# Kernel tuning notes

Hardware: AMD Instinct MI355X
Metric: run time of the kernel (lower is better)

## Reference

```python
import jax, jax.numpy as jnp
import numpy as np

B, T, C, H = 4, 4096, 1024, 16


def setup_inputs() -> dict:
    key = jax.random.key(0)
    k1, k2, k3 = jax.random.split(key, 3)
    x = jax.random.normal(k1, (B, T, C), dtype=jnp.float32)
    # nn.Linear(d_model, 3*d_model, bias=False): weight shape [3C, C]
    W_qkv = jax.random.normal(k2, (3 * C, C), dtype=jnp.float32) * 0.02
    # output Linear(d_model, d_model): weight [C, C], bias [C]
    W_out = jax.random.normal(k3, (C, C), dtype=jnp.float32) * 0.02
    b_out = jnp.zeros((C,), dtype=jnp.float32)
    return {"x": x, "W_qkv": W_qkv, "W_out": W_out, "b_out": b_out}


def reference(x, W_qkv, W_out, b_out):
    Bs, Ts, Cs = x.shape
    dh = Cs // H
    scale = dh ** (-0.5)
    # qkv projection: [B,T,3C]
    qkv = x @ W_qkv.T
    q, k, v = jnp.split(qkv, 3, axis=-1)

    def to_heads(t):  # [B,T,C] -> [B,H,T,dh]
        return t.reshape(Bs, Ts, H, dh).transpose(0, 2, 1, 3)

    q, k, v = to_heads(q), to_heads(k), to_heads(v)
    # rfft over the sequence dim -> [B,H,F,dh], F = T//2+1 (complex64)
    q_f = jnp.fft.rfft(q, axis=-2)
    k_f = jnp.fft.rfft(k, axis=-2)
    # spectral score: sum over head_dim of conj(q)*k, real part -> [B,H,F]
    attn = jnp.sum(jnp.conj(q_f) * k_f, axis=-1).real * scale
    attn = jax.nn.softmax(attn, axis=-1)  # softmax over frequency bins
    v_f = jnp.fft.rfft(v, axis=-2)
    out = jnp.fft.irfft(attn[..., None] * v_f, n=Ts, axis=-2)  # [B,H,T,dh]
    out = out.transpose(0, 2, 1, 3).reshape(Bs, Ts, Cs)
    # output projection (dropout is identity in eval)
    return out @ W_out.T + b_out
```

## Files before the change

kernel.cpp:

```cpp
#include <hip/hip_runtime.h>
#include <math.h>

#define Bsz   4
#define Tsz   4096
#define Csz   1024
#define Hn    16
#define DHn   64
#define NTOT  (Bsz * Tsz)
#define M3    (3 * Csz)
#define Fn    2049
#define BHn   (Bsz * Hn)
#define HALFN 8192

typedef __bf16 bf16x8 __attribute__((ext_vector_type(8)));
typedef __bf16 bf16x4 __attribute__((ext_vector_type(4)));
typedef float  f32x4  __attribute__((ext_vector_type(4)));

#define VMCNT(n) asm volatile("s_waitcnt vmcnt(" #n ")" ::: "memory")
#define LGKM0    asm volatile("s_waitcnt lgkmcnt(0)" ::: "memory")

__device__ __forceinline__ void gload_lds16(const void* g, void* l) {
  __builtin_amdgcn_global_load_lds(
      (const __attribute__((address_space(1))) void*)g,
      (__attribute__((address_space(3))) void*)l, 16, 0, 0);
}

__global__ __launch_bounds__(256)
void cvt_hilo_kernel(const float4* __restrict__ in, bf16x4* __restrict__ hi,
                     bf16x4* __restrict__ lo, int n4) {
  int i = blockIdx.x * blockDim.x + threadIdx.x;
  if (i >= n4) return;
  float4 v = in[i];
  bf16x4 h, l;
  h[0] = (__bf16)v.x; h[1] = (__bf16)v.y; h[2] = (__bf16)v.z; h[3] = (__bf16)v.w;
  l[0] = (__bf16)(v.x - (float)h[0]);
  l[1] = (__bf16)(v.y - (float)h[1]);
  l[2] = (__bf16)(v.z - (float)h[2]);
  l[3] = (__bf16)(v.w - (float)h[3]);
  hi[i] = h;
  lo[i] = l;
}

__global__ __launch_bounds__(256)
void transpose_cvt_kernel(const float* __restrict__ src,
                          __bf16* __restrict__ hi, __bf16* __restrict__ lo) {
  __shared__ float tile[64][65];
  const int tid = threadIdx.x;
  const int n0 = blockIdx.x * 64;
  const int c0 = blockIdx.y * 64;
  const int col = tid & 63;
  const int row4 = tid >> 6;
#pragma unroll
  for (int i = 0; i < 16; ++i) {
    const int r = i * 4 + row4;
    tile[r][col] = src[(size_t)(c0 + r) * NTOT + n0 + col];
  }
  __syncthreads();
#pragma unroll
  for (int i = 0; i < 16; ++i) {
    const int n = i * 4 + row4;
    const float v = tile[col][n];
    const __bf16 h = (__bf16)v;
    const __bf16 l = (__bf16)(v - (float)h);
    hi[(size_t)(n0 + n) * Csz + c0 + col] = h;
    lo[(size_t)(n0 + n) * Csz + c0 + col] = l;
  }
}

template<int COLMAP>
__global__ __launch_bounds__(512, 2)
void gemm_8s(const __bf16* __restrict__ Ahi, const __bf16* __restrict__ Alo,
             const __bf16* __restrict__ Bhi, const __bf16* __restrict__ Blo,
             float* __restrict__ C, int ldC, int nbase,
             const float* __restrict__ bias) {
  __shared__ __align__(16) char lds[131072];

  const int tid  = threadIdx.x;
  const int wid  = tid >> 6;
  const int lane = tid & 63;
  const int wm = wid >> 2, wn = wid & 3;

  int bx = blockIdx.x, by = blockIdx.y;
  {
    const int gx = gridDim.x, gy = gridDim.y;
    const int nwg = gx * gy;
    if ((nwg & 7) == 0) {
      const int flat  = by * gx + bx;
      const int chunk = nwg >> 3;
      const int nf    = (flat & 7) * chunk + (flat >> 3);
      if (COLMAP) { bx = nf / gy; by = nf % gy; }
      else        { bx = nf % gx; by = nf / gx; }
    }
  }
  const int m0 = by * 256;
  const int n0 = bx * 256;

  const int r16 = lane & 15;
  const int kc  = lane >> 4;

  const int aq = (wid & 3) + ((wid & 4) ? 4 : 0);
  const int bq = ((wid & 3) << 1) + (wid >> 2);
  const __bf16* gAh = Ahi + (size_t)(m0 + (wid & 3) * 16 + ((wid & 4) ? 128 : 0) + r16) * Csz + kc * 8;
  const __bf16* gAl = Alo + (size_t)(m0 + (wid & 3) * 16 + ((wid & 4) ? 128 : 0) + r16) * Csz + kc * 8;
  const __bf16* gBh = Bhi + (size_t)(n0 + (wid & 3) * 64 + (wid >> 2) * 16 + r16) * Csz + kc * 8;
  const __bf16* gBl = Blo + (size_t)(n0 + (wid & 3) * 64 + (wid >> 2) * 16 + r16) * Csz + kc * 8;

  auto stA = [&](int h, int ts, char* slot) {
    const size_t o = (size_t)h * 64 * Csz + ts * 32;
    gload_lds16(gAh + o, slot + aq * 1024);
    gload_lds16(gAl + o, slot + 8192 + aq * 1024);
  };
  auto stB = [&](int h, int ts, char* slot) {
    const size_t o = (size_t)h * 32 * Csz + ts * 32;
    gload_lds16(gBh + o, slot + bq * 1024);
    gload_lds16(gBl + o, slot + 8192 + bq * 1024);
  };

  f32x4 acc[8][4];
#pragma unroll
  for (int i = 0; i < 8; ++i)
#pragma unroll
    for (int j = 0; j < 4; ++j) acc[i][j] = (f32x4)(0.f);

  stA(0, 0, lds);            stB(0, 0, lds + 16384);
  stB(1, 0, lds + 32768);    stA(1, 0, lds + 49152);
  stA(0, 1, lds + 65536);    stB(0, 1, lds + 81920);

#pragma unroll 1
  for (int t = 0; t < 32; ++t) {
    char* cur = lds + ((t & 1) << 16);
    char* nxt = lds + (((t & 1) ^ 1) << 16);
    bf16x8 ah[4], al[4], bh[4], bl[4];

    if (t < 31) { VMCNT(8); } else { VMCNT(4); }
    __builtin_amdgcn_s_barrier();
#pragma unroll
    for (int f = 0; f < 4; ++f) {
      const int off = (wm * 4 + f) * 1024 + lane * 16;
      ah[f] = *(const bf16x8*)(cur + off);
      al[f] = *(const bf16x8*)(cur + 8192 + off);
    }
#pragma unroll
    for (int j = 0; j < 2; ++j) {
      const int off = ((wn << 1) + j) * 1024 + lane * 16;
      bh[j] = *(const bf16x8*)(cur + 16384 + off);
      bl[j] = *(const bf16x8*)(cur + 16384 + 8192 + off);
    }
    if (t < 31) stB(1, t + 1, nxt + 32768);
    LGKM0;
    __builtin_amdgcn_sched_barrier(0);
    __builtin_amdgcn_s_setprio(1);
#pragma unroll
    for (int f = 0; f < 4; ++f)
#pragma unroll
      for (int j = 0; j < 2; ++j) {
        f32x4 a_ = acc[f][j];
        a_ = __builtin_amdgcn_mfma_f32_16x16x32_bf16(ah[f], bh[j], a_, 0, 0, 0);
        a_ = __builtin_amdgcn_mfma_f32_16x16x32_bf16(ah[f], bl[j], a_, 0, 0, 0);
        a_ = __builtin_amdgcn_mfma_f32_16x16x32_bf16(al[f], bh[j], a_, 0, 0, 0);
        acc[f][j] = a_;
      }
    __builtin_amdgcn_s_setprio(0);

    if (t < 31) { VMCNT(8); } else { VMCNT(2); }
    __builtin_amdgcn_s_barrier();
#pragma unroll
    for (int j = 0; j < 2; ++j) {
      const int off = ((wn << 1) + j) * 1024 + lane * 16;
      bh[2 + j] = *(const bf16x8*)(cur + 32768 + off);
      bl[2 + j] = *(const bf16x8*)(cur + 32768 + 8192 + off);
    }
    if (t < 31) stA(1, t + 1, nxt + 49152);
    LGKM0;
    __builtin_amdgcn_sched_barrier(0);
    __builtin_amdgcn_s_setprio(1);
#pragma unroll
    for (int f = 0; f < 4; ++f)
#pragma unroll
      for (int j = 0; j < 2; ++j) {
        f32x4 a_ = acc[f][2 + j];
        a_ = __builtin_amdgcn_mfma_f32_16x16x32_bf16(ah[f], bh[2 + j], a_, 0, 0, 0);
        a_ = __builtin_amdgcn_mfma_f32_16x16x32_bf16(ah[f], bl[2 + j], a_, 0, 0, 0);
        a_ = __builtin_amdgcn_mfma_f32_16x16x32_bf16(al[f], bh[2 + j], a_, 0, 0, 0);
        acc[f][2 + j] = a_;
      }
    __builtin_amdgcn_s_setprio(0);

    if (t < 31) { VMCNT(8); } else { VMCNT(0); }
    __builtin_amdgcn_s_barrier();
#pragma unroll
    for (int f = 0; f < 4; ++f) {
      const int off = (wm * 4 + f) * 1024 + lane * 16;
      ah[f] = *(const bf16x8*)(cur + 49152 + off);
      al[f] = *(const bf16x8*)(cur + 49152 + 8192 + off);
    }
    if (t < 30) stA(0, t + 2, cur);
    LGKM0;
    __builtin_amdgcn_sched_barrier(0);
    __builtin_amdgcn_s_setprio(1);
#pragma unroll
    for (int f = 0; f < 4; ++f)
#pragma unroll
      for (int j = 0; j < 2; ++j) {
        f32x4 a_ = acc[4 + f][j];
        a_ = __builtin_amdgcn_mfma_f32_16x16x32_bf16(ah[f], bh[j], a_, 0, 0, 0);
        a_ = __builtin_amdgcn_mfma_f32_16x16x32_bf16(ah[f], bl[j], a_, 0, 0, 0);
        a_ = __builtin_amdgcn_mfma_f32_16x16x32_bf16(al[f], bh[j], a_, 0, 0, 0);
        acc[4 + f][j] = a_;
      }
    __builtin_amdgcn_s_setprio(0);

    __builtin_amdgcn_s_barrier();
    if (t < 30) stB(0, t + 2, cur + 16384);
    __builtin_amdgcn_s_setprio(1);
#pragma unroll
    for (int f = 0; f < 4; ++f)
#pragma unroll
      for (int j = 0; j < 2; ++j) {
        f32x4 a_ = acc[4 + f][2 + j];
        a_ = __builtin_amdgcn_mfma_f32_16x16x32_bf16(ah[f], bh[2 + j], a_, 0, 0, 0);
        a_ = __builtin_amdgcn_mfma_f32_16x16x32_bf16(ah[f], bl[2 + j], a_, 0, 0, 0);
        a_ = __builtin_amdgcn_mfma_f32_16x16x32_bf16(al[f], bh[2 + j], a_, 0, 0, 0);
        acc[4 + f][2 + j] = a_;
      }
    __builtin_amdgcn_s_setprio(0);
  }

  const int cm = m0 + wm * 128 + (lane >> 4) * 4;
  const int cn = nbase + n0 + wn * 64 + (lane & 15);
  float bb[4];
#pragma unroll
  for (int g = 0; g < 4; ++g) bb[g] = bias ? bias[cn - nbase + g * 16] : 0.f;
#pragma unroll
  for (int fm = 0; fm < 8; ++fm)
#pragma unroll
    for (int r = 0; r < 4; ++r) {
      float* cp = C + (size_t)(cm + fm * 16 + r) * ldC + cn;
#pragma unroll
      for (int g = 0; g < 4; ++g) cp[g * 16] = acc[fm][g][r] + bb[g];
    }
}

template<int MF>
__global__ __launch_bounds__(512, 2)
void gemm_8p(const __bf16* __restrict__ Ahi, const __bf16* __restrict__ Alo,
             const __bf16* __restrict__ Bhi, const __bf16* __restrict__ Blo,
             float* __restrict__ C, int ldC, int nbase,
             const float* __restrict__ bias, int colmap) {
  constexpr int BM  = 32 * MF;
  constexpr int SA  = BM * 64;
  constexpr int SB  = 16384;
  constexpr int BUF = 2 * SA + 2 * SB;
  __shared__ __align__(16) char lds[2 * BUF];

  const int tid  = threadIdx.x;
  const int wid  = tid >> 6;
  const int lane = tid & 63;
  const int wm = wid >> 2, wn = wid & 3;

  int bx = blockIdx.x, by = blockIdx.y;
  {
    const int gx = gridDim.x, gy = gridDim.y;
    const int nwg = gx * gy;
    if ((nwg & 7) == 0) {
      const int flat  = by * gx + bx;
      const int chunk = nwg >> 3;
      const int nf    = (flat & 7) * chunk + (flat >> 3);
      if (colmap) { bx = nf / gy; by = nf % gy; }
      else        { bx = nf % gx; by = nf / gx; }
    }
  }
  const int m0 = by * BM;
  const int n0 = bx * 256;

  const int r16 = lane & 15;
  const int kc  = lane >> 4;

  const __bf16* gAh0 = Ahi + (size_t)(m0 + wid * 16 + r16) * Csz + kc * 8;
  const __bf16* gAl0 = Alo + (size_t)(m0 + wid * 16 + r16) * Csz + kc * 8;
  const __bf16* gBh0 = Bhi + (size_t)(n0 + wid * 16 + r16) * Csz + kc * 8;
  const __bf16* gBl0 = Blo + (size_t)(n0 + wid * 16 + r16) * Csz + kc * 8;
  const __bf16* gBh1 = gBh0 + (size_t)128 * Csz;
  const __bf16* gBl1 = gBl0 + (size_t)128 * Csz;
  const int dW = wid * 1024;

  f32x4 acc[MF][4];
#pragma unroll
  for (int i = 0; i < MF; ++i)
#pragma unroll
    for (int j = 0; j < 4; ++j) acc[i][j] = (f32x4)(0.f);

  auto stage = [&](char* base, int k0) {
    gload_lds16(gAh0 + k0, base + dW);
    gload_lds16(gAl0 + k0, base + SA + dW);
    gload_lds16(gBh0 + k0, base + 2 * SA + dW);
    gload_lds16(gBh1 + k0, base + 2 * SA + dW + 8192);
    gload_lds16(gBl0 + k0, base + 2 * SA + SB + dW);
    gload_lds16(gBl1 + k0, base + 2 * SA + SB + dW + 8192);
  };

  stage(lds, 0);

  for (int t = 0; t < 32; ++t) {
    char* buf = lds + (t & 1) * BUF;
    VMCNT(0);
    __builtin_amdgcn_s_barrier();
    if (t < 31) stage(lds + ((t & 1) ^ 1) * BUF, (t + 1) * 32);

#pragma unroll
    for (int mh = 0; mh < 2; ++mh) {
      bf16x8 ah[MF / 2], al[MF / 2];
#pragma unroll
      for (int f = 0; f < MF / 2; ++f) {
        const int off = (wm * MF + mh * (MF / 2) + f) * 1024 + lane * 16;
        ah[f] = *(const bf16x8*)(buf + off);
        al[f] = *(const bf16x8*)(buf + SA + off);
      }
#pragma unroll
      for (int nh = 0; nh < 2; ++nh) {
        bf16x8 bh[2], bl[2];
#pragma unroll
        for (int g = 0; g < 2; ++g) {
          const int off = (wn * 4 + nh * 2 + g) * 1024 + lane * 16;
          bh[g] = *(const bf16x8*)(buf + 2 * SA + off);
          bl[g] = *(const bf16x8*)(buf + 2 * SA + SB + off);
        }
        LGKM0;
        __builtin_amdgcn_sched_barrier(0);
        __builtin_amdgcn_s_setprio(1);
#pragma unroll
        for (int f = 0; f < MF / 2; ++f)
#pragma unroll
          for (int g = 0; g < 2; ++g) {
            f32x4 a_ = acc[mh * (MF / 2) + f][nh * 2 + g];
            a_ = __builtin_amdgcn_mfma_f32_16x16x32_bf16(ah[f], bh[g], a_, 0, 0, 0);
            a_ = __builtin_amdgcn_mfma_f32_16x16x32_bf16(ah[f], bl[g], a_, 0, 0, 0);
            a_ = __builtin_amdgcn_mfma_f32_16x16x32_bf16(al[f], bh[g], a_, 0, 0, 0);
            acc[mh * (MF / 2) + f][nh * 2 + g] = a_;
          }
        __builtin_amdgcn_s_setprio(0);
        __builtin_amdgcn_s_barrier();
      }
    }
  }

  const int cm = m0 + wm * (MF * 16) + (lane >> 4) * 4;
  const int cn = nbase + n0 + wn * 64 + (lane & 15);
  float bb[4];
#pragma unroll
  for (int g = 0; g < 4; ++g) bb[g] = bias ? bias[cn - nbase + g * 16] : 0.f;
#pragma unroll
  for (int fm = 0; fm < MF; ++fm)
#pragma unroll
    for (int r = 0; r < 4; ++r) {
      float* cp = C + (size_t)(cm + fm * 16 + r) * ldC + cn;
#pragma unroll
      for (int g = 0; g < 4; ++g) cp[g * 16] = acc[fm][g][r] + bb[g];
    }
}

template<int NT>
__device__ __forceinline__ void build_twiddle(float2* tw, int tid) {
  const float k = 6.28318530717958647692f / 4096.0f;
#pragma unroll
  for (int i = 0; i < 1024 / NT; ++i) {
    const int e = tid + i * NT;
    float sn, cs;
    __sincosf(k * (float)e, &sn, &cs);
    tw[e] = make_float2(cs, sn);
  }
}

__device__ __forceinline__ float2 cmul(float2 a, float2 b) {
  return make_float2(a.x * b.x - a.y * b.y, a.x * b.y + a.y * b.x);
}

template<int NT>
__device__ __forceinline__ void fft4096_r4(float2* X, float2* Y,
                                           const float2* __restrict__ tw,
                                           int tid, float sign) {
  float2* src = X;
  float2* dst = Y;
#pragma unroll 1
  for (int stage = 0; stage < 6; ++stage) {
    const int s = 1 << (2 * stage);
    __syncthreads();
#pragma unroll
    for (int it = 0; it < 1024 / NT; ++it) {
      const int idx = tid + it * NT;
      const int sp = idx & ~(s - 1);
      float2 a0 = src[idx];
      float2 a1 = src[idx + 1024];
      float2 a2 = src[idx + 2048];
      float2 a3 = src[idx + 3072];
      float2 b0 = make_float2(a0.x + a2.x, a0.y + a2.y);
      float2 b1 = make_float2(a0.x - a2.x, a0.y - a2.y);
      float2 b2 = make_float2(a1.x + a3.x, a1.y + a3.y);
      float2 b3 = make_float2(a1.x - a3.x, a1.y - a3.y);
      float2 y0 = make_float2(b0.x + b2.x, b0.y + b2.y);
      float2 y2 = make_float2(b0.x - b2.x, b0.y - b2.y);
      float2 y1 = make_float2(b1.x - sign * b3.y, b1.y + sign * b3.x);
      float2 y3 = make_float2(b1.x + sign * b3.y, b1.y - sign * b3.x);
      float2 w1 = tw[sp];
      w1.y *= sign;
      float2 w2 = make_float2(w1.x * w1.x - w1.y * w1.y, 2.f * w1.x * w1.y);
      float2 w3 = cmul(w1, w2);
      const int o = idx + 3 * sp;
      dst[o]         = y0;
      dst[o + s]     = cmul(w1, y1);
      dst[o + 2 * s] = cmul(w2, y2);
      dst[o + 3 * s] = cmul(w3, y3);
    }
    float2* t = src; src = dst; dst = t;
  }
  __syncthreads();
}

__global__ __launch_bounds__(512)
void qk_cross_kernel(const float* __restrict__ qkT, float* __restrict__ attn_raw,
                     int bhbase) {
  __shared__ float2 bufA[4096];
  __shared__ float2 bufB[4096];
  __shared__ float2 twid[1024];
  const int tid = threadIdx.x;
  const int blk = blockIdx.x;
  const int d = blk & 63;
  const int bh = bhbase + (blk >> 6);
  const int h = bh & 15;
  const int b = bh >> 4;

  build_twiddle<512>(twid, tid);

  const float4* qrow = (const float4*)(qkT + (size_t)(h * DHn + d) * NTOT + b * Tsz);
  const float4* krow = (const float4*)(qkT + (size_t)(Csz + h * DHn + d) * NTOT + b * Tsz);
#pragma unroll
  for (int i = 0; i < 2; ++i) {
    const int t4 = tid + (i << 9);
    float4 qv = qrow[t4];
    float4 kv = krow[t4];
    bufA[t4 * 4 + 0] = make_float2(qv.x, kv.x);
    bufA[t4 * 4 + 1] = make_float2(qv.y, kv.y);
    bufA[t4 * 4 + 2] = make_float2(qv.z, kv.z);
    bufA[t4 * 4 + 3] = make_float2(qv.w, kv.w);
  }

  fft4096_r4<512>(bufA, bufB, twid, tid, -1.0f);

  float* outp = attn_raw + (size_t)bh * Fn;
  for (int f = tid; f < Fn; f += 512) {
    float2 zf = bufA[f];
    float2 zn = bufA[(4096 - f) & 4095];
    float ar = zf.x + zn.x;
    float ai = zf.y - zn.y;
    float br = zf.x - zn.x;
    float bi = zf.y + zn.y;
    float val = 0.03125f * (ar * bi - ai * br);
    atomicAdd(&outp[f], val);
  }
}

__global__ __launch_bounds__(256)
void softmax_kernel(const float* __restrict__ raw, float* __restrict__ attn) {
  __shared__ float red[256];
  const int tid = threadIdx.x;
  const float* in = raw + (size_t)blockIdx.x * Fn;
  float* outp = attn + (size_t)blockIdx.x * Fn;

  float lmax = -3.4e38f;
  for (int f = tid; f < Fn; f += 256) lmax = fmaxf(lmax, in[f]);
  red[tid] = lmax;
  __syncthreads();
  for (int off = 128; off > 0; off >>= 1) {
    if (tid < off) red[tid] = fmaxf(red[tid], red[tid + off]);
    __syncthreads();
  }
  const float mx = red[0];
  __syncthreads();

  float lsum = 0.f;
  for (int f = tid; f < Fn; f += 256) lsum += __expf(in[f] - mx);
  red[tid] = lsum;
  __syncthreads();
  for (int off = 128; off > 0; off >>= 1) {
    if (tid < off) red[tid] += red[tid + off];
    __syncthreads();
  }
  const float inv = 1.0f / red[0];
  for (int f = tid; f < Fn; f += 256) outp[f] = __expf(in[f] - mx) * inv;
}

__global__ __launch_bounds__(512)
void v_filter_kernel(const float* __restrict__ vT, float* __restrict__ vbarT,
                     const float* __restrict__ attn) {
  __shared__ float2 bufA[4096];
  __shared__ float2 bufB[4096];
  __shared__ float2 twid[1024];
  const int tid = threadIdx.x;
  const int blk = blockIdx.x;
  const int jp = blk & 31;
  const int bh = blk >> 5;
  const int h = bh & 15;
  const int b = bh >> 4;
  const int d0 = jp * 2;

  build_twiddle<512>(twid, tid);

  const float4* v0 = (const float4*)(vT + (size_t)(h * DHn + d0) * NTOT + b * Tsz);
  const float4* v1 = (const float4*)(vT + (size_t)(h * DHn + d0 + 1) * NTOT + b * Tsz);
#pragma unroll
  for (int i = 0; i < 2; ++i) {
    const int t4 = tid + (i << 9);
    float4 av = v0[t4];
    float4 bv = v1[t4];
    bufA[t4 * 4 + 0] = make_float2(av.x, bv.x);
    bufA[t4 * 4 + 1] = make_float2(av.y, bv.y);
    bufA[t4 * 4 + 2] = make_float2(av.z, bv.z);
    bufA[t4 * 4 + 3] = make_float2(av.w, bv.w);
  }

  fft4096_r4<512>(bufA, bufB, twid, tid, -1.0f);

  const float* a = attn + (size_t)bh * Fn;
  for (int f = tid; f < 4096; f += 512) {
    int fm = (f <= 2048) ? f : (4096 - f);
    float s = a[fm];
    float2 z = bufA[f];
    bufA[f] = make_float2(z.x * s, z.y * s);
  }

  fft4096_r4<512>(bufA, bufB, twid, tid, +1.0f);

  float* y0 = vbarT + (size_t)(h * DHn + d0) * NTOT + b * Tsz;
  float* y1 = y0 + NTOT;
  const float inv = 1.0f / 4096.0f;
  for (int t = tid; t < 4096; t += 512) {
    float2 z = bufA[t];
    y0[t] = z.x * inv;
    y1[t] = z.y * inv;
  }
}

__global__ void zero_kernel(float* __restrict__ p, int n) {
  int i = blockIdx.x * blockDim.x + threadIdx.x;
  if (i < n) p[i] = 0.f;
}

extern "C" void kernel_launch(void* const* d_in, const int* in_sizes, int n_in,
                              void* d_out, int out_size, void* d_ws, size_t ws_size,
                              hipStream_t stream) {
  const float* x    = (const float*)d_in[0];
  const float* Wqkv = (const float*)d_in[1];
  const float* Wout = (const float*)d_in[2];
  const float* bout = (const float*)d_in[3];
  float* out = (float*)d_out;

  char* ws = (char*)d_ws;
  float* qkT      = (float*)ws;
  float* vT       = (float*)ws;
  __bf16* VThi    = (__bf16*)ws;
  __bf16* VTlo    = (__bf16*)(ws + 33554432ull);
  float* vbarT    = (float*)(ws + 67108864ull);
  float* attn_raw = (float*)(ws + 134217728ull);
  float* attn     = (float*)(ws + 134742272ull);
  __bf16* Whi     = (__bf16*)(ws + 135266816ull);
  __bf16* Wlo     = (__bf16*)(ws + 141558272ull);
  __bf16* Xhi     = (__bf16*)(ws + 147849728ull);
  __bf16* Xlo     = (__bf16*)(ws + 164626944ull);
  __bf16* Wouthi  = (__bf16*)(ws + 181404160ull);
  __bf16* Woutlo  = (__bf16*)(ws + 183501312ull);

  const int nraw = BHn * Fn;
  zero_kernel<<<(nraw + 255) / 256, 256, 0, stream>>>(attn_raw, nraw);

  cvt_hilo_kernel<<<3072, 256, 0, stream>>>((const float4*)Wqkv,
                                            (bf16x4*)Whi, (bf16x4*)Wlo, 786432);
  cvt_hilo_kernel<<<1024, 256, 0, stream>>>((const float4*)Wout,
                                            (bf16x4*)Wouthi, (bf16x4*)Woutlo, 262144);

  for (int half = 0; half < 2; ++half) {
    cvt_hilo_kernel<<<8192, 256, 0, stream>>>(
        (const float4*)(x + (size_t)half * HALFN * Csz),
        (bf16x4*)Xhi, (bf16x4*)Xlo, 2097152);
    gemm_8s<1><<<dim3(32, 8), 512, 0, stream>>>(Whi, Wlo, Xhi, Xlo,
                                                qkT, NTOT, half * HALFN, nullptr);
    qk_cross_kernel<<<2048, 512, 0, stream>>>(qkT, attn_raw, half * 32);
    gemm_8p<4><<<dim3(32, 8), 512, 0, stream>>>(Whi + 2048 * Csz, Wlo + 2048 * Csz,
                                                Xhi, Xlo, vT, NTOT, half * HALFN,
                                                nullptr, 1);
  }

  softmax_kernel<<<BHn, 256, 0, stream>>>(attn_raw, attn);

  v_filter_kernel<<<2048, 512, 0, stream>>>(vT, vbarT, attn);

  transpose_cvt_kernel<<<dim3(NTOT / 64, Csz / 64), 256, 0, stream>>>(vbarT, VThi, VTlo);

  gemm_8s<0><<<dim3(4, 64), 512, 0, stream>>>(VThi, VTlo, Wouthi, Woutlo,
                                              out, Csz, 0, bout);
}
```

Measured before the change: 567.2 us.

## Rewrite V-projection GEMM as 4-quadrant staged pipeline with partial vmcnt waits

Replaces the double-buffered gemm_8p (one full-tile stage per k-step with vmcnt(0)) with gemm_8s4, which splits each 128x256 tile into A/B halves loaded into separate LDS slots. It issues loads for the next step's quadrants between MFMA phases and waits with vmcnt(6) instead of draining all loads. The goal is to hide global-to-LDS latency behind MFMA work in the V projection GEMM. The cost is more barriers per k-step and tighter, more fragile wait-count bookkeeping.

```diff
diff --git a/kernel.cpp b/kernel.cpp
--- a/kernel.cpp
+++ b/kernel.cpp
@@ -241,17 +241,13 @@
     }
 }
 
-template<int MF>
+template<int COLMAP>
 __global__ __launch_bounds__(512, 2)
-void gemm_8p(const __bf16* __restrict__ Ahi, const __bf16* __restrict__ Alo,
-             const __bf16* __restrict__ Bhi, const __bf16* __restrict__ Blo,
-             float* __restrict__ C, int ldC, int nbase,
-             const float* __restrict__ bias, int colmap) {
-  constexpr int BM  = 32 * MF;
-  constexpr int SA  = BM * 64;
-  constexpr int SB  = 16384;
-  constexpr int BUF = 2 * SA + 2 * SB;
-  __shared__ __align__(16) char lds[2 * BUF];
+void gemm_8s4(const __bf16* __restrict__ Ahi, const __bf16* __restrict__ Alo,
+              const __bf16* __restrict__ Bhi, const __bf16* __restrict__ Blo,
+              float* __restrict__ C, int ldC, int nbase,
+              const float* __restrict__ bias) {
+  __shared__ __align__(16) char lds[98304];
 
   const int tid  = threadIdx.x;
   const int wid  = tid >> 6;
@@ -266,91 +262,150 @@
       const int flat  = by * gx + bx;
       const int chunk = nwg >> 3;
       const int nf    = (flat & 7) * chunk + (flat >> 3);
-      if (colmap) { bx = nf / gy; by = nf % gy; }
+      if (COLMAP) { bx = nf / gy; by = nf % gy; }
       else        { bx = nf % gx; by = nf / gx; }
     }
   }
-  const int m0 = by * BM;
+  const int m0 = by * 128;
   const int n0 = bx * 256;
 
   const int r16 = lane & 15;
   const int kc  = lane >> 4;
 
-  const __bf16* gAh0 = Ahi + (size_t)(m0 + wid * 16 + r16) * Csz + kc * 8;
-  const __bf16* gAl0 = Alo + (size_t)(m0 + wid * 16 + r16) * Csz + kc * 8;
-  const __bf16* gBh0 = Bhi + (size_t)(n0 + wid * 16 + r16) * Csz + kc * 8;
-  const __bf16* gBl0 = Blo + (size_t)(n0 + wid * 16 + r16) * Csz + kc * 8;
-  const __bf16* gBh1 = gBh0 + (size_t)128 * Csz;
-  const __bf16* gBl1 = gBl0 + (size_t)128 * Csz;
-  const int dW = wid * 1024;
-
-  f32x4 acc[MF][4];
-#pragma unroll
-  for (int i = 0; i < MF; ++i)
+  const int cw = wid & 3;
+  const __bf16* gA = ((wid & 4) ? Alo : Ahi) +
+      (size_t)(m0 + (cw >> 1) * 64 + (cw & 1) * 16 + r16) * Csz + kc * 8;
+  const int adst = ((wid & 4) ? 4096 : 0) + cw * 1024;
+  const int bq = ((wid & 3) << 1) + (wid >> 2);
+  const __bf16* gBh = Bhi + (size_t)(n0 + (wid & 3) * 64 + (wid >> 2) * 16 + r16) * Csz + kc * 8;
+  const __bf16* gBl = Blo + (size_t)(n0 + (wid & 3) * 64 + (wid >> 2) * 16 + r16) * Csz + kc * 8;
+
+  auto stA = [&](int h, int ts, char* slot) {
+    gload_lds16(gA + (size_t)h * 32 * Csz + ts * 32, slot + adst);
+  };
+  auto stB = [&](int h, int ts, char* slot) {
+    const size_t o = (size_t)h * 32 * Csz + ts * 32;
+    gload_lds16(gBh + o, slot + bq * 1024);
+    gload_lds16(gBl + o, slot + 8192 + bq * 1024);
+  };
+
+  f32x4 acc[4][4];
+#pragma unroll
+  for (int i = 0; i < 4; ++i)
 #pragma unroll
     for (int j = 0; j < 4; ++j) acc[i][j] = (f32x4)(0.f);
 
-  auto stage = [&](char* base, int k0) {
-    gload_lds16(gAh0 + k0, base + dW);
-    gload_lds16(gAl0 + k0, base + SA + dW);
-    gload_lds16(gBh0 + k0, base + 2 * SA + dW);
-    gload_lds16(gBh1 + k0, base + 2 * SA + dW + 8192);
-    gload_lds16(gBl0 + k0, base + 2 * SA + SB + dW);
-    gload_lds16(gBl1 + k0, base + 2 * SA + SB + dW + 8192);
-  };
-
-  stage(lds, 0);
-
+  stA(0, 0, lds);            stB(0, 0, lds + 8192);
+  stB(1, 0, lds + 24576);    stA(1, 0, lds + 40960);
+  stA(0, 1, lds + 49152);    stB(0, 1, lds + 49152 + 8192);
+
+#pragma unroll 1
   for (int t = 0; t < 32; ++t) {
-    char* buf = lds + (t & 1) * BUF;
-    VMCNT(0);
-    __builtin_amdgcn_s_barrier();
-    if (t < 31) stage(lds + ((t & 1) ^ 1) * BUF, (t + 1) * 32);
-
-#pragma unroll
-    for (int mh = 0; mh < 2; ++mh) {
-      bf16x8 ah[MF / 2], al[MF / 2];
-#pragma unroll
-      for (int f = 0; f < MF / 2; ++f) {
-        const int off = (wm * MF + mh * (MF / 2) + f) * 1024 + lane * 16;
-        ah[f] = *(const bf16x8*)(buf + off);
-        al[f] = *(const bf16x8*)(buf + SA + off);
-      }
-#pragma unroll
-      for (int nh = 0; nh < 2; ++nh) {
-        bf16x8 bh[2], bl[2];
-#pragma unroll
-        for (int g = 0; g < 2; ++g) {
-          const int off = (wn * 4 + nh * 2 + g) * 1024 + lane * 16;
-          bh[g] = *(const bf16x8*)(buf + 2 * SA + off);
-          bl[g] = *(const bf16x8*)(buf + 2 * SA + SB + off);
-        }
-        LGKM0;
-        __builtin_amdgcn_sched_barrier(0);
-        __builtin_amdgcn_s_setprio(1);
-#pragma unroll
-        for (int f = 0; f < MF / 2; ++f)
-#pragma unroll
-          for (int g = 0; g < 2; ++g) {
-            f32x4 a_ = acc[mh * (MF / 2) + f][nh * 2 + g];
-            a_ = __builtin_amdgcn_mfma_f32_16x16x32_bf16(ah[f], bh[g], a_, 0, 0, 0);
-            a_ = __builtin_amdgcn_mfma_f32_16x16x32_bf16(ah[f], bl[g], a_, 0, 0, 0);
-            a_ = __builtin_amdgcn_mfma_f32_16x16x32_bf16(al[f], bh[g], a_, 0, 0, 0);
-            acc[mh * (MF / 2) + f][nh * 2 + g] = a_;
-          }
-        __builtin_amdgcn_s_setprio(0);
-        __builtin_amdgcn_s_barrier();
-      }
-    }
-  }
-
-  const int cm = m0 + wm * (MF * 16) + (lane >> 4) * 4;
+    char* cur = lds + (t & 1) * 49152;
+    char* nxt = lds + ((t & 1) ^ 1) * 49152;
+    bf16x8 ah[2], al[2], bh[4], bl[4];
+
+    if (t < 31) { VMCNT(6); } else { VMCNT(3); }
+    __builtin_amdgcn_s_barrier();
+#pragma unroll
+    for (int f = 0; f < 2; ++f) {
+      const int off = (wm * 2 + f) * 1024 + lane * 16;
+      ah[f] = *(const bf16x8*)(cur + off);
+      al[f] = *(const bf16x8*)(cur + 4096 + off);
+    }
+#pragma unroll
+    for (int j = 0; j < 2; ++j) {
+      const int off = ((wn << 1) + j) * 1024 + lane * 16;
+      bh[j] = *(const bf16x8*)(cur + 8192 + off);
+      bl[j] = *(const bf16x8*)(cur + 8192 + 8192 + off);
+    }
+    if (t < 31) stB(1, t + 1, nxt + 24576);
+    LGKM0;
+    __builtin_amdgcn_sched_barrier(0);
+    __builtin_amdgcn_s_setprio(1);
+#pragma unroll
+    for (int f = 0; f < 2; ++f)
+#pragma unroll
+      for (int j = 0; j < 2; ++j) {
+        f32x4 a_ = acc[f][j];
+        a_ = __builtin_amdgcn_mfma_f32_16x16x32_bf16(ah[f], bh[j], a_, 0, 0, 0);
+        a_ = __builtin_amdgcn_mfma_f32_16x16x32_bf16(ah[f], bl[j], a_, 0, 0, 0);
+        a_ = __builtin_amdgcn_mfma_f32_16x16x32_bf16(al[f], bh[j], a_, 0, 0, 0);
+        acc[f][j] = a_;
+      }
+    __builtin_amdgcn_s_setprio(0);
+
+    if (t < 31) { VMCNT(6); } else { VMCNT(1); }
+    __builtin_amdgcn_s_barrier();
+#pragma unroll
+    for (int j = 0; j < 2; ++j) {
+      const int off = ((wn << 1) + j) * 1024 + lane * 16;
+      bh[2 + j] = *(const bf16x8*)(cur + 24576 + off);
+      bl[2 + j] = *(const bf16x8*)(cur + 24576 + 8192 + off);
+    }
+    if (t < 31) stA(1, t + 1, nxt + 40960);
+    LGKM0;
+    __builtin_amdgcn_sched_barrier(0);
+    __builtin_amdgcn_s_setprio(1);
+#pragma unroll
+    for (int f = 0; f < 2; ++f)
+#pragma unroll
+      for (int j = 0; j < 2; ++j) {
+        f32x4 a_ = acc[f][2 + j];
+        a_ = __builtin_amdgcn_mfma_f32_16x16x32_bf16(ah[f], bh[2 + j], a_, 0, 0, 0);
+        a_ = __builtin_amdgcn_mfma_f32_16x16x32_bf16(ah[f], bl[2 + j], a_, 0, 0, 0);
+        a_ = __builtin_amdgcn_mfma_f32_16x16x32_bf16(al[f], bh[2 + j], a_, 0, 0, 0);
+        acc[f][2 + j] = a_;
+      }
+    __builtin_amdgcn_s_setprio(0);
+
+    if (t < 31) { VMCNT(6); } else { VMCNT(0); }
+    __builtin_amdgcn_s_barrier();
+#pragma unroll
+    for (int f = 0; f < 2; ++f) {
+      const int off = (wm * 2 + f) * 1024 + lane * 16;
+      ah[f] = *(const bf16x8*)(cur + 40960 + off);
+      al[f] = *(const bf16x8*)(cur + 40960 + 4096 + off);
+    }
+    if (t < 30) stA(0, t + 2, cur);
+    LGKM0;
+    __builtin_amdgcn_sched_barrier(0);
+    __builtin_amdgcn_s_setprio(1);
+#pragma unroll
+    for (int f = 0; f < 2; ++f)
+#pragma unroll
+      for (int j = 0; j < 2; ++j) {
+        f32x4 a_ = acc[2 + f][j];
+        a_ = __builtin_amdgcn_mfma_f32_16x16x32_bf16(ah[f], bh[j], a_, 0, 0, 0);
+        a_ = __builtin_amdgcn_mfma_f32_16x16x32_bf16(ah[f], bl[j], a_, 0, 0, 0);
+        a_ = __builtin_amdgcn_mfma_f32_16x16x32_bf16(al[f], bh[j], a_, 0, 0, 0);
+        acc[2 + f][j] = a_;
+      }
+    __builtin_amdgcn_s_setprio(0);
+
+    __builtin_amdgcn_s_barrier();
+    if (t < 30) stB(0, t + 2, cur + 8192);
+    __builtin_amdgcn_s_setprio(1);
+#pragma unroll
+    for (int f = 0; f < 2; ++f)
+#pragma unroll
+      for (int j = 0; j < 2; ++j) {
+        f32x4 a_ = acc[2 + f][2 + j];
+        a_ = __builtin_amdgcn_mfma_f32_16x16x32_bf16(ah[f], bh[2 + j], a_, 0, 0, 0);
+        a_ = __builtin_amdgcn_mfma_f32_16x16x32_bf16(ah[f], bl[2 + j], a_, 0, 0, 0);
+        a_ = __builtin_amdgcn_mfma_f32_16x16x32_bf16(al[f], bh[2 + j], a_, 0, 0, 0);
+        acc[2 + f][2 + j] = a_;
+      }
+    __builtin_amdgcn_s_setprio(0);
+  }
+
+  const int cm = m0 + wm * 64 + (lane >> 4) * 4;
   const int cn = nbase + n0 + wn * 64 + (lane & 15);
   float bb[4];
 #pragma unroll
   for (int g = 0; g < 4; ++g) bb[g] = bias ? bias[cn - nbase + g * 16] : 0.f;
 #pragma unroll
-  for (int fm = 0; fm < MF; ++fm)
+  for (int fm = 0; fm < 4; ++fm)
 #pragma unroll
     for (int r = 0; r < 4; ++r) {
       float* cp = C + (size_t)(cm + fm * 16 + r) * ldC + cn;
@@ -584,9 +639,9 @@
     gemm_8s<1><<<dim3(32, 8), 512, 0, stream>>>(Whi, Wlo, Xhi, Xlo,
                                                 qkT, NTOT, half * HALFN, nullptr);
     qk_cross_kernel<<<2048, 512, 0, stream>>>(qkT, attn_raw, half * 32);
-    gemm_8p<4><<<dim3(32, 8), 512, 0, stream>>>(Whi + 2048 * Csz, Wlo + 2048 * Csz,
-                                                Xhi, Xlo, vT, NTOT, half * HALFN,
-                                                nullptr, 1);
+    gemm_8s4<1><<<dim3(32, 8), 512, 0, stream>>>(Whi + 2048 * Csz, Wlo + 2048 * Csz,
+                                                 Xhi, Xlo, vT, NTOT, half * HALFN,
+                                                 nullptr);
   }
 
   softmax_kernel<<<BHn, 256, 0, stream>>>(attn_raw, attn);
```

Measured after the change: 553.7 us. 2.4% less time.
